# Optimization experiments

Hardware: AMD Instinct MI355X
Metric: run time of the kernel (lower is better)

The kernel has to match this reference:

```python
import jax, jax.numpy as jnp
from jax import lax
import numpy as np


def _laplacian_kernel():
    # 7-point 3D Laplacian stencil, OIDHW layout [1,1,3,3,3]
    k = np.zeros((1, 1, 3, 3, 3), dtype=np.float32)
    k[0, 0, 1, 1, 1] = -6.0
    k[0, 0, 1, 1, 0] = 1.0
    k[0, 0, 1, 1, 2] = 1.0
    k[0, 0, 1, 0, 1] = 1.0
    k[0, 0, 1, 2, 1] = 1.0
    k[0, 0, 0, 1, 1] = 1.0
    k[0, 0, 2, 1, 1] = 1.0
    return jnp.asarray(k)


def setup_inputs() -> dict:
    key = jax.random.key(0)
    k1, k2 = jax.random.split(key)
    shape = (1, 1, 160, 160, 160)  # NCDHW tumor-concentration grid
    c_init = jax.random.uniform(k1, shape, dtype=jnp.float32)
    therapy_map = jax.random.uniform(k2, shape, dtype=jnp.float32)
    return {
        "c_init": c_init,
        "D": jnp.float32(0.1),      # diffusivity
        "rho": jnp.float32(0.5),    # proliferation rate
        "dt": jnp.float32(1.0),     # total time window
        "therapy_map": therapy_map,
        "steps": 30,
    }


def reference(c_init, D, rho, dt, therapy_map, steps):
    kern = _laplacian_kernel()
    delta_t = dt / steps

    def step(c, _):
        lap = lax.conv_general_dilated(
            c, kern, window_strides=(1, 1, 1), padding="SAME",
            dimension_numbers=("NCDHW", "OIDHW", "NCDHW"))
        growth = D * lap + rho * c * (1.0 - c)
        kill = therapy_map * c * 2.0
        c = jnp.clip(c + (growth - kill) * delta_t, 0.0, 1.0)
        return c, None

    c, _ = lax.scan(step, c_init, None, length=steps)
    return c
```

## Files before the change

kernel.cpp:

```cpp
#include <hip/hip_runtime.h>


#define NX 160
#define NY 160
#define NZ 160
#define NXQ (NX / 4)
#define NPLANE (NX * NY)
#define NGROUPS (NZ * NY * NXQ)

#define CT_BS 256
#define CT_NTHREADS (NGROUPS / 4)
#define CT_NBLOCKS (CT_NTHREADS / CT_BS)
#define BPQ 25

typedef float f32x4 __attribute__((ext_vector_type(4)));

__device__ unsigned int g_flag[CT_NBLOCKS * 16];
__device__ unsigned int g_xcdmap[CT_NBLOCKS];
__device__ __align__(16) float g_mid[NGROUPS * 4];

#define GLD4(dst, voff, base, flg) \
    asm volatile("global_load_dwordx4 %0, %1, %2" flg \
                 : "=v"(dst) : "v"(voff), "s"(base))
#define GLD1(dst, voff, base, flg) \
    asm volatile("global_load_dword %0, %1, %2" flg \
                 : "=v"(dst) : "v"(voff), "s"(base))
#define GST4(voff, val, base, flg) \
    asm volatile("global_store_dwordx4 %0, %1, %2" flg \
                 :: "v"(voff), "v"(val), "s"(base) : "memory")

__device__ __forceinline__ f32x4 ld4v(const float* p) {
    return *reinterpret_cast<const f32x4*>(p);
}

__device__ __forceinline__ f32x4 step_cell(
    f32x4 cc, f32x4 ym, f32x4 yp, f32x4 zm, f32x4 zp,
    float xl, float xr, f32x4 tm, float D, float rho, float delta_t)
{
    f32x4 o;
    float lap, g;
    lap = xl    + cc[1] + ym[0] + yp[0] + zm[0] + zp[0] - 6.f * cc[0];
    g   = D * lap + rho * cc[0] * (1.f - cc[0]) - 2.f * tm[0] * cc[0];
    o[0] = fminf(fmaxf(cc[0] + g * delta_t, 0.f), 1.f);
    lap = cc[0] + cc[2] + ym[1] + yp[1] + zm[1] + zp[1] - 6.f * cc[1];
    g   = D * lap + rho * cc[1] * (1.f - cc[1]) - 2.f * tm[1] * cc[1];
    o[1] = fminf(fmaxf(cc[1] + g * delta_t, 0.f), 1.f);
    lap = cc[1] + cc[3] + ym[2] + yp[2] + zm[2] + zp[2] - 6.f * cc[2];
    g   = D * lap + rho * cc[2] * (1.f - cc[2]) - 2.f * tm[2] * cc[2];
    o[2] = fminf(fmaxf(cc[2] + g * delta_t, 0.f), 1.f);
    lap = cc[2] + xr    + ym[3] + yp[3] + zm[3] + zp[3] - 6.f * cc[3];
    g   = D * lap + rho * cc[3] * (1.f - cc[3]) - 2.f * tm[3] * cc[3];
    o[3] = fminf(fmaxf(cc[3] + g * delta_t, 0.f), 1.f);
    return o;
}

__global__ __launch_bounds__(CT_BS, 4) void therapy_all(
    const float* __restrict__ c_init,
    const float* __restrict__ ther,
    float* __restrict__ out,
    float* __restrict__ ws,
    const float* __restrict__ Dp,
    const float* __restrict__ rhop,
    const float* __restrict__ dtp,
    const int* __restrict__ stepsp)
{
    __shared__ float2 lx[4][CT_BS];

    const int lb = (blockIdx.x & 7) * (CT_NBLOCKS / 8) + (blockIdx.x >> 3);
    const int tx = threadIdx.x;
    const int tid = lb * CT_BS + tx;

    const int xq = tid % NXQ;
    const int t2 = tid / NXQ;
    const int y  = t2 % NY;
    const int q  = lb / BPQ;

    const int   steps   = *stepsp;
    const float D       = *Dp;
    const float rho     = *rhop;
    const float delta_t = *dtp / (float)steps;

    const unsigned int fbase =
        __hip_atomic_load(&g_flag[lb * 16], __ATOMIC_RELAXED,
                          __HIP_MEMORY_SCOPE_AGENT);

    const int  offym = (y > 0)        ? -NX : 0;
    const int  offyp = (y < NY - 1)   ?  NX : 0;
    const int  offxl = (xq > 0)       ? -1  : 0;
    const bool mym = (y == 0), myp = (y == NY - 1);
    const bool mxl = (xq == 0), mxr = (xq == NXQ - 1);
    const bool mzm = (q == 0);
    const bool mzp = (q == 39);

    const int b0 = ((4 * q) * NY + y) * NX + 4 * xq;
    const int b3 = b0 + 3 * NPLANE;

    const unsigned o_c  = (unsigned)b0 * 4u;
    const unsigned o_ym = (unsigned)(b0 + offym) * 4u;
    const unsigned o_yp = (unsigned)(b0 + offyp) * 4u;
    const unsigned o_xl = (unsigned)(b0 + offxl) * 4u;
    const unsigned o_xr = (unsigned)(b0 + (mxr ? 3 : 4)) * 4u;
    const unsigned o_zm = (unsigned)(b0 + (mzm ? 0 : -NPLANE)) * 4u;
    const unsigned o_zp = (unsigned)(b3 + (mzp ? 0 :  NPLANE)) * 4u;

    f32x4 tv[4], cv[4];
#pragma unroll
    for (int p = 0; p < 4; ++p) {
        tv[p] = ld4v(ther   + b0 + p * NPLANE);
        cv[p] = ld4v(c_init + b0 + p * NPLANE);
    }

    unsigned int myx;
    asm volatile("s_getreg_b32 %0, hwreg(HW_REG_XCC_ID)" : "=s"(myx));
    if (tx == 0) {
        __hip_atomic_store(&g_xcdmap[lb], myx, __ATOMIC_RELAXED,
                           __HIP_MEMORY_SCOPE_AGENT);
        asm volatile("s_waitcnt vmcnt(0)" ::: "memory");
        __hip_atomic_store(&g_flag[lb * 16], fbase + 1u, __ATOMIC_RELAXED,
                           __HIP_MEMORY_SCOPE_AGENT);
    }
    if (tx < 4) {
        const int d = (tx == 0) ? -BPQ : (tx == 1) ? -1 : (tx == 2) ? 1 : BPQ;
        int nb = lb + d;
        nb = nb < 0 ? 0 : (nb >= CT_NBLOCKS ? CT_NBLOCKS - 1 : nb);
        while (__hip_atomic_load(&g_flag[nb * 16], __ATOMIC_RELAXED,
                                 __HIP_MEMORY_SCOPE_AGENT) < fbase + 1u) {
            __builtin_amdgcn_s_sleep(2);
        }
    }
    __syncthreads();

    #define MAPLD(b) __hip_atomic_load(&g_xcdmap[(b)], __ATOMIC_RELAXED, \
                                       __HIP_MEMORY_SCOPE_AGENT)
    const unsigned xm25 = (lb >= BPQ)              ? MAPLD(lb - BPQ) : myx;
    const unsigned xm1  = (lb >= 1)                ? MAPLD(lb - 1)   : myx;
    const unsigned xp1  = (lb < CT_NBLOCKS - 1)    ? MAPLD(lb + 1)   : myx;
    const unsigned xp25 = (lb < CT_NBLOCKS - BPQ)  ? MAPLD(lb + BPQ) : myx;

    const bool zmX = (xm25 != myx);
    const bool zpX = (xp25 != myx);
    const bool ymX = (tx < NXQ)          && (xm1 != myx);
    const bool ypX = (tx >= CT_BS - NXQ) && (xp1 != myx);
    const bool xlX = (tx == 0)           && (xm1 != myx);
    const bool xrX = (tx == CT_BS - 1)   && (xp1 != myx);
    const bool stYX = (tx < NXQ && xm1 != myx) ||
                      (tx >= CT_BS - NXQ && xp1 != myx);
    const bool st0X = stYX || zmX;
    const bool st3X = stYX || zpX;

    const int OFF = (3 - (steps - 1) % 3) % 3;

    const float* rd = c_init;
    for (int i = 0; i < steps; ++i) {
        const int s = (i + OFF) % 3;
        float* wr = (s == 0) ? out : (s == 1) ? ws : g_mid;

#pragma unroll
        for (int p = 0; p < 4; ++p)
            lx[p][tx] = make_float2(cv[p][0], cv[p][3]);

        if (i > 0 && tx < 4) {
            const int d = (tx == 0) ? -BPQ : (tx == 1) ? -1
                        : (tx == 2) ?    1 : BPQ;
            int nb = lb + d;
            nb = nb < 0 ? 0 : (nb >= CT_NBLOCKS ? CT_NBLOCKS - 1 : nb);
            const unsigned tgt = fbase + 1u + (unsigned)i;
            while (__hip_atomic_load(&g_flag[nb * 16], __ATOMIC_RELAXED,
                                     __HIP_MEMORY_SCOPE_AGENT) < tgt) {
                __builtin_amdgcn_s_sleep(2);
            }
        }
        __syncthreads();

        f32x4 ym[4], yp[4], zmg, zpg;
#pragma unroll
        for (int p = 0; p < 4; ++p) {
            const unsigned po = (unsigned)(p * NPLANE * 4);
            if (ymX) { GLD4(ym[p], o_ym + po, rd, " sc1"); }
            else     { GLD4(ym[p], o_ym + po, rd, " sc0"); }
            if (ypX) { GLD4(yp[p], o_yp + po, rd, " sc1"); }
            else     { GLD4(yp[p], o_yp + po, rd, " sc0"); }
        }
        if (zmX) { GLD4(zmg, o_zm, rd, " sc1"); } else { GLD4(zmg, o_zm, rd, " sc0"); }
        if (zpX) { GLD4(zpg, o_zp, rd, " sc1"); } else { GLD4(zpg, o_zp, rd, " sc0"); }
        float xl[4], xr[4];
        if (tx == 0) {
#pragma unroll
            for (int p = 0; p < 4; ++p) {
                const unsigned po = (unsigned)(p * NPLANE * 4);
                if (xlX) { GLD1(xl[p], o_xl + po, rd, " sc1"); }
                else     { GLD1(xl[p], o_xl + po, rd, " sc0"); }
            }
        } else {
#pragma unroll
            for (int p = 0; p < 4; ++p) xl[p] = lx[p][tx - 1].y;
        }
        if (tx == CT_BS - 1) {
#pragma unroll
            for (int p = 0; p < 4; ++p) {
                const unsigned po = (unsigned)(p * NPLANE * 4);
                if (xrX) { GLD1(xr[p], o_xr + po, rd, " sc1"); }
                else     { GLD1(xr[p], o_xr + po, rd, " sc0"); }
            }
        } else {
#pragma unroll
            for (int p = 0; p < 4; ++p) xr[p] = lx[p][tx + 1].x;
        }
        asm volatile("s_waitcnt vmcnt(0)" ::: "memory");
        __builtin_amdgcn_sched_barrier(0);

        const f32x4 z4 = {0.f, 0.f, 0.f, 0.f};
        if (mym) {
#pragma unroll
            for (int p = 0; p < 4; ++p) ym[p] = z4;
        }
        if (myp) {
#pragma unroll
            for (int p = 0; p < 4; ++p) yp[p] = z4;
        }
        if (mzm) zmg = z4;
        if (mzp) zpg = z4;
        if (mxl) {
#pragma unroll
            for (int p = 0; p < 4; ++p) xl[p] = 0.f;
        }
        if (mxr) {
#pragma unroll
            for (int p = 0; p < 4; ++p) xr[p] = 0.f;
        }

        f32x4 n[4];
        n[0] = step_cell(cv[0], ym[0], yp[0], zmg,   cv[1], xl[0], xr[0], tv[0], D, rho, delta_t);
        n[1] = step_cell(cv[1], ym[1], yp[1], cv[0], cv[2], xl[1], xr[1], tv[1], D, rho, delta_t);
        n[2] = step_cell(cv[2], ym[2], yp[2], cv[1], cv[3], xl[2], xr[2], tv[2], D, rho, delta_t);
        n[3] = step_cell(cv[3], ym[3], yp[3], cv[2], zpg,   xl[3], xr[3], tv[3], D, rho, delta_t);

        if (st0X) { GST4(o_c, n[0], wr, " sc1"); } else { GST4(o_c, n[0], wr, ""); }
        if (stYX) { GST4(o_c + 102400u, n[1], wr, " sc1"); }
        else      { GST4(o_c + 102400u, n[1], wr, ""); }
        if (stYX) { GST4(o_c + 204800u, n[2], wr, " sc1"); }
        else      { GST4(o_c + 204800u, n[2], wr, ""); }
        if (st3X) { GST4(o_c + 307200u, n[3], wr, " sc1"); }
        else      { GST4(o_c + 307200u, n[3], wr, ""); }

        __syncthreads();
        if (tx == 0) {
            __hip_atomic_store(&g_flag[lb * 16], fbase + 2u + (unsigned)i,
                               __ATOMIC_RELAXED, __HIP_MEMORY_SCOPE_AGENT);
        }

#pragma unroll
        for (int p = 0; p < 4; ++p) cv[p] = n[p];
        rd = wr;
    }
}

extern "C" void kernel_launch(void* const* d_in, const int* in_sizes, int n_in,
                              void* d_out, int out_size, void* d_ws, size_t ws_size,
                              hipStream_t stream) {
    const float* c_init = (const float*)d_in[0];
    const float* Dp     = (const float*)d_in[1];
    const float* rhop   = (const float*)d_in[2];
    const float* dtp    = (const float*)d_in[3];
    const float* ther   = (const float*)d_in[4];
    const int*   stepsp = (const int*)d_in[5];

    float* out = (float*)d_out;
    float* wsA = (float*)d_ws;

    therapy_all<<<dim3(CT_NBLOCKS), dim3(CT_BS), 0, stream>>>(
        c_init, ther, out, wsA, Dp, rhop, dtp, stepsp);
}
```

Before: 251.7 us.

## Halve z-planes per thread to double persistent blocks and occupancy

Each thread now updates two z-planes instead of four, doubling the number of persistent co-resident blocks and raising launch bounds to eight blocks per CU. This trades register-level reuse of z-neighbours for more wavefronts in flight, aiming to hide memory and flag-sync latency in each timestep. It adds extra z-halo loads per cell and twice as many inter-block flags to poll, and relies on all 2000 blocks remaining co-resident for the spin-wait scheme.

```diff
diff --git a/kernel.cpp b/kernel.cpp
--- a/kernel.cpp
+++ b/kernel.cpp
@@ -9,9 +9,9 @@
 #define NGROUPS (NZ * NY * NXQ)
 
 #define CT_BS 256
-#define CT_NTHREADS (NGROUPS / 4)
+#define CT_NTHREADS (NGROUPS / 2)
 #define CT_NBLOCKS (CT_NTHREADS / CT_BS)
-#define BPQ 25
+#define BPK 25
 
 typedef float f32x4 __attribute__((ext_vector_type(4)));
 
@@ -54,7 +54,7 @@
     return o;
 }
 
-__global__ __launch_bounds__(CT_BS, 4) void therapy_all(
+__global__ __launch_bounds__(CT_BS, 8) void therapy_all(
     const float* __restrict__ c_init,
     const float* __restrict__ ther,
     float* __restrict__ out,
@@ -64,7 +64,7 @@
     const float* __restrict__ dtp,
     const int* __restrict__ stepsp)
 {
-    __shared__ float2 lx[4][CT_BS];
+    __shared__ float2 lx[2][CT_BS];
 
     const int lb = (blockIdx.x & 7) * (CT_NBLOCKS / 8) + (blockIdx.x >> 3);
     const int tx = threadIdx.x;
@@ -73,7 +73,7 @@
     const int xq = tid % NXQ;
     const int t2 = tid / NXQ;
     const int y  = t2 % NY;
-    const int q  = lb / BPQ;
+    const int k  = lb / BPK;
 
     const int   steps   = *stepsp;
     const float D       = *Dp;
@@ -89,11 +89,11 @@
     const int  offxl = (xq > 0)       ? -1  : 0;
     const bool mym = (y == 0), myp = (y == NY - 1);
     const bool mxl = (xq == 0), mxr = (xq == NXQ - 1);
-    const bool mzm = (q == 0);
-    const bool mzp = (q == 39);
-
-    const int b0 = ((4 * q) * NY + y) * NX + 4 * xq;
-    const int b3 = b0 + 3 * NPLANE;
+    const bool mzm = (k == 0);
+    const bool mzp = (k == NZ / 2 - 1);
+
+    const int b0 = ((2 * k) * NY + y) * NX + 4 * xq;
+    const int b1 = b0 + NPLANE;
 
     const unsigned o_c  = (unsigned)b0 * 4u;
     const unsigned o_ym = (unsigned)(b0 + offym) * 4u;
@@ -101,14 +101,12 @@
     const unsigned o_xl = (unsigned)(b0 + offxl) * 4u;
     const unsigned o_xr = (unsigned)(b0 + (mxr ? 3 : 4)) * 4u;
     const unsigned o_zm = (unsigned)(b0 + (mzm ? 0 : -NPLANE)) * 4u;
-    const unsigned o_zp = (unsigned)(b3 + (mzp ? 0 :  NPLANE)) * 4u;
-
-    f32x4 tv[4], cv[4];
-#pragma unroll
-    for (int p = 0; p < 4; ++p) {
-        tv[p] = ld4v(ther   + b0 + p * NPLANE);
-        cv[p] = ld4v(c_init + b0 + p * NPLANE);
-    }
+    const unsigned o_zp = (unsigned)(b1 + (mzp ? 0 :  NPLANE)) * 4u;
+
+    const f32x4 tv0 = ld4v(ther + b0);
+    const f32x4 tv1 = ld4v(ther + b1);
+    f32x4 cv0 = ld4v(c_init + b0);
+    f32x4 cv1 = ld4v(c_init + b1);
 
     unsigned int myx;
     asm volatile("s_getreg_b32 %0, hwreg(HW_REG_XCC_ID)" : "=s"(myx));
@@ -120,7 +118,7 @@
                            __HIP_MEMORY_SCOPE_AGENT);
     }
     if (tx < 4) {
-        const int d = (tx == 0) ? -BPQ : (tx == 1) ? -1 : (tx == 2) ? 1 : BPQ;
+        const int d = (tx == 0) ? -BPK : (tx == 1) ? -1 : (tx == 2) ? 1 : BPK;
         int nb = lb + d;
         nb = nb < 0 ? 0 : (nb >= CT_NBLOCKS ? CT_NBLOCKS - 1 : nb);
         while (__hip_atomic_load(&g_flag[nb * 16], __ATOMIC_RELAXED,
@@ -132,10 +130,10 @@
 
     #define MAPLD(b) __hip_atomic_load(&g_xcdmap[(b)], __ATOMIC_RELAXED, \
                                        __HIP_MEMORY_SCOPE_AGENT)
-    const unsigned xm25 = (lb >= BPQ)              ? MAPLD(lb - BPQ) : myx;
+    const unsigned xm25 = (lb >= BPK)              ? MAPLD(lb - BPK) : myx;
     const unsigned xm1  = (lb >= 1)                ? MAPLD(lb - 1)   : myx;
     const unsigned xp1  = (lb < CT_NBLOCKS - 1)    ? MAPLD(lb + 1)   : myx;
-    const unsigned xp25 = (lb < CT_NBLOCKS - BPQ)  ? MAPLD(lb + BPQ) : myx;
+    const unsigned xp25 = (lb < CT_NBLOCKS - BPK)  ? MAPLD(lb + BPK) : myx;
 
     const bool zmX = (xm25 != myx);
     const bool zpX = (xp25 != myx);
@@ -146,7 +144,7 @@
     const bool stYX = (tx < NXQ && xm1 != myx) ||
                       (tx >= CT_BS - NXQ && xp1 != myx);
     const bool st0X = stYX || zmX;
-    const bool st3X = stYX || zpX;
+    const bool st1X = stYX || zpX;
 
     const int OFF = (3 - (steps - 1) % 3) % 3;
 
@@ -155,13 +153,12 @@
         const int s = (i + OFF) % 3;
         float* wr = (s == 0) ? out : (s == 1) ? ws : g_mid;
 
-#pragma unroll
-        for (int p = 0; p < 4; ++p)
-            lx[p][tx] = make_float2(cv[p][0], cv[p][3]);
+        lx[0][tx] = make_float2(cv0[0], cv0[3]);
+        lx[1][tx] = make_float2(cv1[0], cv1[3]);
 
         if (i > 0 && tx < 4) {
-            const int d = (tx == 0) ? -BPQ : (tx == 1) ? -1
-                        : (tx == 2) ?    1 : BPQ;
+            const int d = (tx == 0) ? -BPK : (tx == 1) ? -1
+                        : (tx == 2) ?    1 : BPK;
             int nb = lb + d;
             nb = nb < 0 ? 0 : (nb >= CT_NBLOCKS ? CT_NBLOCKS - 1 : nb);
             const unsigned tgt = fbase + 1u + (unsigned)i;
@@ -172,76 +169,41 @@
         }
         __syncthreads();
 
-        f32x4 ym[4], yp[4], zmg, zpg;
-#pragma unroll
-        for (int p = 0; p < 4; ++p) {
-            const unsigned po = (unsigned)(p * NPLANE * 4);
-            if (ymX) { GLD4(ym[p], o_ym + po, rd, " sc1"); }
-            else     { GLD4(ym[p], o_ym + po, rd, " sc0"); }
-            if (ypX) { GLD4(yp[p], o_yp + po, rd, " sc1"); }
-            else     { GLD4(yp[p], o_yp + po, rd, " sc0"); }
-        }
+        f32x4 ym0, ym1, yp0, yp1, zmg, zpg;
+        if (ymX) { GLD4(ym0, o_ym, rd, " sc1"); GLD4(ym1, o_ym + 102400u, rd, " sc1"); }
+        else     { GLD4(ym0, o_ym, rd, " sc0"); GLD4(ym1, o_ym + 102400u, rd, " sc0"); }
+        if (ypX) { GLD4(yp0, o_yp, rd, " sc1"); GLD4(yp1, o_yp + 102400u, rd, " sc1"); }
+        else     { GLD4(yp0, o_yp, rd, " sc0"); GLD4(yp1, o_yp + 102400u, rd, " sc0"); }
         if (zmX) { GLD4(zmg, o_zm, rd, " sc1"); } else { GLD4(zmg, o_zm, rd, " sc0"); }
         if (zpX) { GLD4(zpg, o_zp, rd, " sc1"); } else { GLD4(zpg, o_zp, rd, " sc0"); }
-        float xl[4], xr[4];
+        float xl0, xl1, xr0, xr1;
         if (tx == 0) {
-#pragma unroll
-            for (int p = 0; p < 4; ++p) {
-                const unsigned po = (unsigned)(p * NPLANE * 4);
-                if (xlX) { GLD1(xl[p], o_xl + po, rd, " sc1"); }
-                else     { GLD1(xl[p], o_xl + po, rd, " sc0"); }
-            }
-        } else {
-#pragma unroll
-            for (int p = 0; p < 4; ++p) xl[p] = lx[p][tx - 1].y;
-        }
+            if (xlX) { GLD1(xl0, o_xl, rd, " sc1"); GLD1(xl1, o_xl + 102400u, rd, " sc1"); }
+            else     { GLD1(xl0, o_xl, rd, " sc0"); GLD1(xl1, o_xl + 102400u, rd, " sc0"); }
+        } else { xl0 = lx[0][tx - 1].y; xl1 = lx[1][tx - 1].y; }
         if (tx == CT_BS - 1) {
-#pragma unroll
-            for (int p = 0; p < 4; ++p) {
-                const unsigned po = (unsigned)(p * NPLANE * 4);
-                if (xrX) { GLD1(xr[p], o_xr + po, rd, " sc1"); }
-                else     { GLD1(xr[p], o_xr + po, rd, " sc0"); }
-            }
-        } else {
-#pragma unroll
-            for (int p = 0; p < 4; ++p) xr[p] = lx[p][tx + 1].x;
-        }
+            if (xrX) { GLD1(xr0, o_xr, rd, " sc1"); GLD1(xr1, o_xr + 102400u, rd, " sc1"); }
+            else     { GLD1(xr0, o_xr, rd, " sc0"); GLD1(xr1, o_xr + 102400u, rd, " sc0"); }
+        } else { xr0 = lx[0][tx + 1].x; xr1 = lx[1][tx + 1].x; }
         asm volatile("s_waitcnt vmcnt(0)" ::: "memory");
         __builtin_amdgcn_sched_barrier(0);
 
         const f32x4 z4 = {0.f, 0.f, 0.f, 0.f};
-        if (mym) {
-#pragma unroll
-            for (int p = 0; p < 4; ++p) ym[p] = z4;
-        }
-        if (myp) {
-#pragma unroll
-            for (int p = 0; p < 4; ++p) yp[p] = z4;
-        }
+        if (mym) { ym0 = z4; ym1 = z4; }
+        if (myp) { yp0 = z4; yp1 = z4; }
         if (mzm) zmg = z4;
         if (mzp) zpg = z4;
-        if (mxl) {
-#pragma unroll
-            for (int p = 0; p < 4; ++p) xl[p] = 0.f;
-        }
-        if (mxr) {
-#pragma unroll
-            for (int p = 0; p < 4; ++p) xr[p] = 0.f;
-        }
-
-        f32x4 n[4];
-        n[0] = step_cell(cv[0], ym[0], yp[0], zmg,   cv[1], xl[0], xr[0], tv[0], D, rho, delta_t);
-        n[1] = step_cell(cv[1], ym[1], yp[1], cv[0], cv[2], xl[1], xr[1], tv[1], D, rho, delta_t);
-        n[2] = step_cell(cv[2], ym[2], yp[2], cv[1], cv[3], xl[2], xr[2], tv[2], D, rho, delta_t);
-        n[3] = step_cell(cv[3], ym[3], yp[3], cv[2], zpg,   xl[3], xr[3], tv[3], D, rho, delta_t);
-
-        if (st0X) { GST4(o_c, n[0], wr, " sc1"); } else { GST4(o_c, n[0], wr, ""); }
-        if (stYX) { GST4(o_c + 102400u, n[1], wr, " sc1"); }
-        else      { GST4(o_c + 102400u, n[1], wr, ""); }
-        if (stYX) { GST4(o_c + 204800u, n[2], wr, " sc1"); }
-        else      { GST4(o_c + 204800u, n[2], wr, ""); }
-        if (st3X) { GST4(o_c + 307200u, n[3], wr, " sc1"); }
-        else      { GST4(o_c + 307200u, n[3], wr, ""); }
+        if (mxl) { xl0 = 0.f; xl1 = 0.f; }
+        if (mxr) { xr0 = 0.f; xr1 = 0.f; }
+
+        const f32x4 n0 = step_cell(cv0, ym0, yp0, zmg, cv1, xl0, xr0, tv0,
+                                   D, rho, delta_t);
+        const f32x4 n1 = step_cell(cv1, ym1, yp1, cv0, zpg, xl1, xr1, tv1,
+                                   D, rho, delta_t);
+
+        if (st0X) { GST4(o_c, n0, wr, " sc1"); } else { GST4(o_c, n0, wr, ""); }
+        if (st1X) { GST4(o_c + 102400u, n1, wr, " sc1"); }
+        else      { GST4(o_c + 102400u, n1, wr, ""); }
 
         __syncthreads();
         if (tx == 0) {
@@ -249,8 +211,8 @@
                                __ATOMIC_RELAXED, __HIP_MEMORY_SCOPE_AGENT);
         }
 
-#pragma unroll
-        for (int p = 0; p < 4; ++p) cv[p] = n[p];
+        cv0 = n0;
+        cv1 = n1;
         rd = wr;
     }
 }
```

Result: slower. 296.3 us (+17.7%).
